# Kernel tuning notes

Measured on AMD Instinct MI355X. Metric: run time of the kernel, lower is better.

## Reference

```python
import jax, jax.numpy as jnp
import numpy as np

ALPHA = 0.2
NEG_INF = -9e15


def setup_inputs() -> dict:
    key = jax.random.key(0)
    k1, k2, k3, k4 = jax.random.split(key, 4)
    B, N, Fin, Fout = 8, 2048, 128, 64
    h = jax.random.normal(k1, (B, N, Fin), dtype=jnp.float32)
    adj = jax.random.randint(k2, (N, N), 0, 2, dtype=jnp.int32)
    # xavier-uniform-ish scale for params
    W = jax.random.normal(k3, (Fin, Fout), dtype=jnp.float32) * (1.414 * (2.0 / (Fin + Fout)) ** 0.5)
    a = jax.random.normal(k4, (2 * Fout, 1), dtype=jnp.float32) * (1.414 * (2.0 / (2 * Fout + 1)) ** 0.5)
    return {"h": h, "adj": adj, "W": W, "a": a}


def reference(h, adj, W, a):
    # h: [B,N,Fin], adj: [N,N] int, W: [Fin,Fout], a: [2*Fout,1]
    Wh = jnp.matmul(h, W)                       # [B,N,F]
    Fout = W.shape[1]
    a1 = a[:Fout, 0]                            # attends to source node i
    a2 = a[Fout:, 0]                            # attends to target node j
    # e[b,i,j] = leakyrelu(Wh[b,i]·a1 + Wh[b,j]·a2)  (no [B,N,N,2F] tensor)
    si = jnp.einsum('bnf,f->bn', Wh, a1)        # [B,N]
    sj = jnp.einsum('bnf,f->bn', Wh, a2)        # [B,N]
    e = si[:, :, None] + sj[:, None, :]         # [B,N,N]
    e = jnp.where(e > 0, e, ALPHA * e)          # leaky_relu
    mask = (adj > 0)[None, :, :]                # [1,N,N] broadcast over batch
    attention = jax.nn.softmax(jnp.where(mask, e, NEG_INF), axis=2)
    h_prime = jnp.matmul(attention, Wh)         # [B,N,F]
    return jax.nn.elu(h_prime), attention
```

## Files before the change

### kernel.cpp

```cpp
#include <hip/hip_runtime.h>
#include <hip/hip_bf16.h>
#include <string.h>

constexpr int B_ = 8;
constexpr int N_ = 2048;
constexpr int FIN = 128;
constexpr int FOUT = 64;
constexpr float ALPHA_ = 0.2f;
constexpr float NEG_INF_ = -9000000000000000.0f;

typedef __attribute__((ext_vector_type(8))) short bf16x8;
typedef __attribute__((ext_vector_type(4))) float f32x4;

static __device__ __forceinline__ unsigned short f2bf(float x) {
  unsigned int u = __float_as_uint(x);
  unsigned int r = u + 0x7fffu + ((u >> 16) & 1u);
  return (unsigned short)(r >> 16);
}

__global__ __launch_bounds__(256) void k_wh(
    const float* __restrict__ h, const float* __restrict__ W,
    const float* __restrict__ a, unsigned short* __restrict__ WhT,
    float* __restrict__ si, float* __restrict__ sj) {
  const int lane = threadIdx.x & 63;
  const int wv = threadIdx.x >> 6;
  const int grow0 = blockIdx.x * 32 + wv * 8;
  const int f = lane;
  float acc[8] = {0.f, 0.f, 0.f, 0.f, 0.f, 0.f, 0.f, 0.f};
  const float* hp = h + (size_t)grow0 * FIN;
#pragma unroll 4
  for (int k = 0; k < FIN; k += 4) {
    float w0 = W[k * FOUT + f];
    float w1 = W[(k + 1) * FOUT + f];
    float w2 = W[(k + 2) * FOUT + f];
    float w3 = W[(k + 3) * FOUT + f];
#pragma unroll
    for (int r = 0; r < 8; ++r) {
      float4 hv = *(const float4*)(hp + r * FIN + k);
      acc[r] = fmaf(hv.x, w0, acc[r]);
      acc[r] = fmaf(hv.y, w1, acc[r]);
      acc[r] = fmaf(hv.z, w2, acc[r]);
      acc[r] = fmaf(hv.w, w3, acc[r]);
    }
  }
  const float a1 = a[f], a2 = a[FOUT + f];
#pragma unroll
  for (int r = 0; r < 8; ++r) {
    float p1 = acc[r] * a1;
    float p2 = acc[r] * a2;
#pragma unroll
    for (int off = 32; off; off >>= 1) {
      p1 += __shfl_xor(p1, off);
      p2 += __shfl_xor(p2, off);
    }
    if (lane == 0) {
      si[grow0 + r] = p1;
      sj[grow0 + r] = p2;
    }
  }
  const int b = grow0 >> 11;
  const int n0 = grow0 & (N_ - 1);
  __align__(16) unsigned short u[8];
#pragma unroll
  for (int r = 0; r < 8; ++r) u[r] = f2bf(acc[r]);
  *(bf16x8*)&WhT[(((size_t)(b * FOUT + f)) << 11) + n0] = *(const bf16x8*)u;
}

__global__ __launch_bounds__(256) void k_pack(
    const int* __restrict__ adj, unsigned long long* __restrict__ mask_rm,
    unsigned int* __restrict__ mask_t) {
  const int lane = threadIdx.x & 63;
  const int wv = threadIdx.x >> 6;
  const int r = blockIdx.x * 4 + wv;
  const int* row = adj + (size_t)r * N_;
  unsigned int wacc = 0;
#pragma unroll
  for (int it = 0; it < 32; ++it) {
    int v = row[it * 64 + lane];
    unsigned long long bm = __ballot(v > 0);
    if (lane == 0) mask_rm[r * 32 + it] = bm;
    wacc |= ((unsigned int)(v > 0)) << it;
  }
  mask_t[r * 64 + lane] = wacc;
}

__global__ __launch_bounds__(256) void k_stats(
    const unsigned int* __restrict__ mask_t, const float* __restrict__ si,
    const float* __restrict__ sj, float* __restrict__ mrow,
    float* __restrict__ rrow) {
  const int lane = threadIdx.x & 63;
  const int wv = threadIdx.x >> 6;
  const int row = blockIdx.x * 4 + wv;
  const int b = row >> 11;
  const int i = row & (N_ - 1);
  const unsigned int w32 = mask_t[i * 64 + lane];
  const float* sjb = sj + ((size_t)b << 11);
  float sjv[32];
  float M = -3.0e38f;
#pragma unroll
  for (int it = 0; it < 32; ++it) {
    sjv[it] = sjb[it * 64 + lane];
    if ((w32 >> it) & 1u) M = fmaxf(M, sjv[it]);
  }
#pragma unroll
  for (int off = 32; off; off >>= 1) M = fmaxf(M, __shfl_xor(M, off));
  const float siv = si[row];
  const float e0 = siv + M;
  const float m = e0 > 0.f ? e0 : ALPHA_ * e0;
  float s = 0.f;
#pragma unroll
  for (int it = 0; it < 32; ++it) {
    float e = siv + sjv[it];
    float v = e > 0.f ? e : ALPHA_ * e;
    float p = __expf(v - m);
    s += ((w32 >> it) & 1u) ? p : 0.f;
  }
#pragma unroll
  for (int off = 32; off; off >>= 1) s += __shfl_xor(s, off);
  if (lane == 0) {
    mrow[row] = m;
    rrow[row] = 1.f / s;
  }
}

constexpr int TI = 32;

__global__ __launch_bounds__(512, 4) void k_hp(
    const unsigned short* __restrict__ WhT,
    const unsigned long long* __restrict__ mask_rm,
    const float* __restrict__ si, const float* __restrict__ sjg,
    const float* __restrict__ mrow, const float* __restrict__ rrow,
    float* __restrict__ h_out) {
  __shared__ float red[4][TI][FOUT];

  const int bid = blockIdx.x;
  const int swz = (bid & 7) * 64 + (bid >> 3);
  const int b = swz >> 6;
  const int i0 = (swz & 63) * TI;

  const int tid = threadIdx.x;
  const int lane = tid & 63;
  const int wv = tid >> 6;
  const int rl = lane & 15;
  const int hi = lane >> 4;
  const int jsl = wv * 256;

  const int grow0 = (b << 11) + i0 + rl;
  const int grow1 = grow0 + 16;
  const float sir0 = si[grow0], sir1 = si[grow1];
  const float mK0 = mrow[grow0] * 1.44269504f, mK1 = mrow[grow1] * 1.44269504f;
  const float rr0 = rrow[grow0], rr1 = rrow[grow1];
  const float* __restrict__ sjb = sjg + ((size_t)b << 11);

  const unsigned char* maskb = (const unsigned char*)mask_rm;
  const uint4 mA0 = *(const uint4*)(maskb + (i0 + rl) * 256 + (jsl >> 3));
  const uint4 mA1 = *(const uint4*)(maskb + (i0 + rl) * 256 + (jsl >> 3) + 16);
  const uint4 mB0 = *(const uint4*)(maskb + (i0 + 16 + rl) * 256 + (jsl >> 3));
  const uint4 mB1 = *(const uint4*)(maskb + (i0 + 16 + rl) * 256 + (jsl >> 3) + 16);
  const unsigned int mw0[8] = {mA0.x, mA0.y, mA0.z, mA0.w, mA1.x, mA1.y, mA1.z, mA1.w};
  const unsigned int mw1[8] = {mB0.x, mB0.y, mB0.z, mB0.w, mB1.x, mB1.y, mB1.z, mB1.w};

  const unsigned short* wbp[4];
#pragma unroll
  for (int ct = 0; ct < 4; ++ct)
    wbp[ct] = WhT + (((size_t)(b * FOUT + ct * 16 + rl)) << 11) + jsl + hi * 8;

  f32x4 acc[2][4];
#pragma unroll
  for (int rt = 0; rt < 2; ++rt)
#pragma unroll
    for (int ct = 0; ct < 4; ++ct) acc[rt][ct] = (f32x4){0.f, 0.f, 0.f, 0.f};

#pragma unroll
  for (int ks = 0; ks < 8; ++ks) {
    const int jb = jsl + ks * 32 + hi * 8;
    const float4 s0 = *(const float4*)(sjb + jb);
    const float4 s1 = *(const float4*)(sjb + jb + 4);
    const float sjl[8] = {s0.x, s0.y, s0.z, s0.w, s1.x, s1.y, s1.z, s1.w};

    bf16x8 afr0, afr1;
    {
      const unsigned int mby = (mw0[ks] >> (hi * 8)) & 0xffu;
      __align__(16) unsigned short u[8];
#pragma unroll
      for (int e = 0; e < 8; ++e) {
        float ev = sir0 + sjl[e];
        float v = fmaxf(ev, ALPHA_ * ev);
        float p = exp2f(fmaf(v, 1.44269504f, -mK0)) * rr0;
        u[e] = ((mby >> e) & 1u) ? f2bf(p) : 0;
      }
      afr0 = *(const bf16x8*)u;
    }
    {
      const unsigned int mby = (mw1[ks] >> (hi * 8)) & 0xffu;
      __align__(16) unsigned short u[8];
#pragma unroll
      for (int e = 0; e < 8; ++e) {
        float ev = sir1 + sjl[e];
        float v = fmaxf(ev, ALPHA_ * ev);
        float p = exp2f(fmaf(v, 1.44269504f, -mK1)) * rr1;
        u[e] = ((mby >> e) & 1u) ? f2bf(p) : 0;
      }
      afr1 = *(const bf16x8*)u;
    }

#pragma unroll
    for (int ct = 0; ct < 4; ++ct) {
      bf16x8 bv = *(const bf16x8*)(wbp[ct] + ks * 32);
      acc[0][ct] = __builtin_amdgcn_mfma_f32_16x16x32_bf16(afr0, bv, acc[0][ct], 0, 0, 0);
      acc[1][ct] = __builtin_amdgcn_mfma_f32_16x16x32_bf16(afr1, bv, acc[1][ct], 0, 0, 0);
    }
  }

  if (wv < 4) {
#pragma unroll
    for (int rt = 0; rt < 2; ++rt)
#pragma unroll
      for (int ct = 0; ct < 4; ++ct)
#pragma unroll
        for (int rg = 0; rg < 4; ++rg)
          red[wv][rt * 16 + hi * 4 + rg][ct * 16 + rl] = acc[rt][ct][rg];
  }
  __syncthreads();
  if (wv >= 4) {
#pragma unroll
    for (int rt = 0; rt < 2; ++rt)
#pragma unroll
      for (int ct = 0; ct < 4; ++ct)
#pragma unroll
        for (int rg = 0; rg < 4; ++rg)
          red[wv - 4][rt * 16 + hi * 4 + rg][ct * 16 + rl] += acc[rt][ct][rg];
  }
  __syncthreads();

#pragma unroll
  for (int k = tid; k < TI * FOUT; k += 512) {
    const int r = k >> 6;
    const int c = k & 63;
    float x = red[0][r][c] + red[1][r][c] + red[2][r][c] + red[3][r][c];
    float o = x > 0.f ? x : __expf(x) - 1.f;
    h_out[(((size_t)((b << 11) + i0 + r)) << 6) + c] = o;
  }
}

__global__ __launch_bounds__(256) void k_att(
    const unsigned char* __restrict__ maskb, const float* __restrict__ si,
    const float* __restrict__ sjg, const float* __restrict__ mrow,
    const float* __restrict__ rrow, float* __restrict__ att_out) {
  const int lane = threadIdx.x & 63;
  const int wv = threadIdx.x >> 6;
  const int row = blockIdx.x * 4 + wv;
  const int b = row >> 11;
  const int i = row & (N_ - 1);
  const float sir = si[row];
  const float mK = mrow[row] * 1.44269504f;
  const float rr = rrow[row];
  const float* __restrict__ sjb = sjg + ((size_t)b << 11);
  const unsigned char* __restrict__ mb = maskb + i * 256;
  float* __restrict__ ao = att_out + ((size_t)row << 11);

#pragma unroll
  for (int it = 0; it < 8; ++it) {
    const int j = it * 256 + lane * 4;
    const float4 s = *(const float4*)(sjb + j);
    const unsigned int mby = mb[it * 32 + (lane >> 1)] >> ((lane & 1) * 4);
    const float sjl[4] = {s.x, s.y, s.z, s.w};
    float av[4];
#pragma unroll
    for (int e = 0; e < 4; ++e) {
      float ev = sir + sjl[e];
      float v = fmaxf(ev, ALPHA_ * ev);
      float p = exp2f(fmaf(v, 1.44269504f, -mK)) * rr;
      av[e] = ((mby >> e) & 1u) ? p : 0.f;
    }
    f32x4 vv = {av[0], av[1], av[2], av[3]};
    *(f32x4*)(ao + j) = vv;
  }
}

extern "C" void kernel_launch(void* const* d_in, const int* in_sizes, int n_in,
                              void* d_out, int out_size, void* d_ws, size_t ws_size,
                              hipStream_t stream) {
  const float* h = (const float*)d_in[0];
  const int* adj = (const int*)d_in[1];
  const float* W = (const float*)d_in[2];
  const float* a = (const float*)d_in[3];

  float* out = (float*)d_out;
  float* h_out = out;
  float* att_out = out + (size_t)B_ * N_ * FOUT;

  unsigned short* WhT = (unsigned short*)d_ws;
  float* si = (float*)((char*)d_ws + (size_t)2 * 1024 * 1024);
  float* sj = si + B_ * N_;
  float* mrow = sj + B_ * N_;
  float* rrow = mrow + B_ * N_;
  unsigned long long* mask_rm = (unsigned long long*)(rrow + B_ * N_);
  unsigned int* mask_t = (unsigned int*)((char*)mask_rm + (size_t)N_ * 32 * 8);

  k_wh<<<B_ * N_ / 32, 256, 0, stream>>>(h, W, a, WhT, si, sj);
  k_pack<<<N_ / 4, 256, 0, stream>>>(adj, mask_rm, mask_t);
  k_stats<<<B_ * N_ / 4, 256, 0, stream>>>(mask_t, si, sj, mrow, rrow);
  k_hp<<<B_ * (N_ / TI), 512, 0, stream>>>(WhT, mask_rm, si, sj, mrow, rrow,
                                           h_out);
  k_att<<<B_ * N_ / 4, 256, 0, stream>>>((const unsigned char*)mask_rm, si, sj,
                                         mrow, rrow, att_out);
}
```

Before: 97.96 us.

## Compute h_prime by reading the written attention matrix instead of recomputing probabilities

The fused k_hp kernel, which recomputed masked softmax probabilities on the fly before the MFMA product, is removed. A new k_gemm kernel runs after k_att, reads the fp32 attention output from global memory, converts it to bf16 and multiplies it with WhT. This removes the duplicated exp and mask work but adds a 128 MB read of the attention matrix, which is likely to be served partly from cache, plus a serial dependency on k_att.

```diff
diff --git a/kernel.cpp b/kernel.cpp
--- a/kernel.cpp
+++ b/kernel.cpp
@@ -123,126 +123,6 @@
   }
 }
 
-constexpr int TI = 32;
-
-__global__ __launch_bounds__(512, 4) void k_hp(
-    const unsigned short* __restrict__ WhT,
-    const unsigned long long* __restrict__ mask_rm,
-    const float* __restrict__ si, const float* __restrict__ sjg,
-    const float* __restrict__ mrow, const float* __restrict__ rrow,
-    float* __restrict__ h_out) {
-  __shared__ float red[4][TI][FOUT];
-
-  const int bid = blockIdx.x;
-  const int swz = (bid & 7) * 64 + (bid >> 3);
-  const int b = swz >> 6;
-  const int i0 = (swz & 63) * TI;
-
-  const int tid = threadIdx.x;
-  const int lane = tid & 63;
-  const int wv = tid >> 6;
-  const int rl = lane & 15;
-  const int hi = lane >> 4;
-  const int jsl = wv * 256;
-
-  const int grow0 = (b << 11) + i0 + rl;
-  const int grow1 = grow0 + 16;
-  const float sir0 = si[grow0], sir1 = si[grow1];
-  const float mK0 = mrow[grow0] * 1.44269504f, mK1 = mrow[grow1] * 1.44269504f;
-  const float rr0 = rrow[grow0], rr1 = rrow[grow1];
-  const float* __restrict__ sjb = sjg + ((size_t)b << 11);
-
-  const unsigned char* maskb = (const unsigned char*)mask_rm;
-  const uint4 mA0 = *(const uint4*)(maskb + (i0 + rl) * 256 + (jsl >> 3));
-  const uint4 mA1 = *(const uint4*)(maskb + (i0 + rl) * 256 + (jsl >> 3) + 16);
-  const uint4 mB0 = *(const uint4*)(maskb + (i0 + 16 + rl) * 256 + (jsl >> 3));
-  const uint4 mB1 = *(const uint4*)(maskb + (i0 + 16 + rl) * 256 + (jsl >> 3) + 16);
-  const unsigned int mw0[8] = {mA0.x, mA0.y, mA0.z, mA0.w, mA1.x, mA1.y, mA1.z, mA1.w};
-  const unsigned int mw1[8] = {mB0.x, mB0.y, mB0.z, mB0.w, mB1.x, mB1.y, mB1.z, mB1.w};
-
-  const unsigned short* wbp[4];
-#pragma unroll
-  for (int ct = 0; ct < 4; ++ct)
-    wbp[ct] = WhT + (((size_t)(b * FOUT + ct * 16 + rl)) << 11) + jsl + hi * 8;
-
-  f32x4 acc[2][4];
-#pragma unroll
-  for (int rt = 0; rt < 2; ++rt)
-#pragma unroll
-    for (int ct = 0; ct < 4; ++ct) acc[rt][ct] = (f32x4){0.f, 0.f, 0.f, 0.f};
-
-#pragma unroll
-  for (int ks = 0; ks < 8; ++ks) {
-    const int jb = jsl + ks * 32 + hi * 8;
-    const float4 s0 = *(const float4*)(sjb + jb);
-    const float4 s1 = *(const float4*)(sjb + jb + 4);
-    const float sjl[8] = {s0.x, s0.y, s0.z, s0.w, s1.x, s1.y, s1.z, s1.w};
-
-    bf16x8 afr0, afr1;
-    {
-      const unsigned int mby = (mw0[ks] >> (hi * 8)) & 0xffu;
-      __align__(16) unsigned short u[8];
-#pragma unroll
-      for (int e = 0; e < 8; ++e) {
-        float ev = sir0 + sjl[e];
-        float v = fmaxf(ev, ALPHA_ * ev);
-        float p = exp2f(fmaf(v, 1.44269504f, -mK0)) * rr0;
-        u[e] = ((mby >> e) & 1u) ? f2bf(p) : 0;
-      }
-      afr0 = *(const bf16x8*)u;
-    }
-    {
-      const unsigned int mby = (mw1[ks] >> (hi * 8)) & 0xffu;
-      __align__(16) unsigned short u[8];
-#pragma unroll
-      for (int e = 0; e < 8; ++e) {
-        float ev = sir1 + sjl[e];
-        float v = fmaxf(ev, ALPHA_ * ev);
-        float p = exp2f(fmaf(v, 1.44269504f, -mK1)) * rr1;
-        u[e] = ((mby >> e) & 1u) ? f2bf(p) : 0;
-      }
-      afr1 = *(const bf16x8*)u;
-    }
-
-#pragma unroll
-    for (int ct = 0; ct < 4; ++ct) {
-      bf16x8 bv = *(const bf16x8*)(wbp[ct] + ks * 32);
-      acc[0][ct] = __builtin_amdgcn_mfma_f32_16x16x32_bf16(afr0, bv, acc[0][ct], 0, 0, 0);
-      acc[1][ct] = __builtin_amdgcn_mfma_f32_16x16x32_bf16(afr1, bv, acc[1][ct], 0, 0, 0);
-    }
-  }
-
-  if (wv < 4) {
-#pragma unroll
-    for (int rt = 0; rt < 2; ++rt)
-#pragma unroll
-      for (int ct = 0; ct < 4; ++ct)
-#pragma unroll
-        for (int rg = 0; rg < 4; ++rg)
-          red[wv][rt * 16 + hi * 4 + rg][ct * 16 + rl] = acc[rt][ct][rg];
-  }
-  __syncthreads();
-  if (wv >= 4) {
-#pragma unroll
-    for (int rt = 0; rt < 2; ++rt)
-#pragma unroll
-      for (int ct = 0; ct < 4; ++ct)
-#pragma unroll
-        for (int rg = 0; rg < 4; ++rg)
-          red[wv - 4][rt * 16 + hi * 4 + rg][ct * 16 + rl] += acc[rt][ct][rg];
-  }
-  __syncthreads();
-
-#pragma unroll
-  for (int k = tid; k < TI * FOUT; k += 512) {
-    const int r = k >> 6;
-    const int c = k & 63;
-    float x = red[0][r][c] + red[1][r][c] + red[2][r][c] + red[3][r][c];
-    float o = x > 0.f ? x : __expf(x) - 1.f;
-    h_out[(((size_t)((b << 11) + i0 + r)) << 6) + c] = o;
-  }
-}
-
 __global__ __launch_bounds__(256) void k_att(
     const unsigned char* __restrict__ maskb, const float* __restrict__ si,
     const float* __restrict__ sjg, const float* __restrict__ mrow,
@@ -278,6 +158,79 @@
   }
 }
 
+__global__ __launch_bounds__(512, 4) void k_gemm(
+    const float* __restrict__ att, const unsigned short* __restrict__ WhT,
+    float* __restrict__ h_out) {
+  __shared__ float red[4][16][FOUT];
+
+  const int bid = blockIdx.x;
+  const int swz = (bid & 7) * 64 + (bid >> 3);
+  const int b = swz >> 6;
+  const int i0 = (swz & 63) * 32;
+
+  const int tid = threadIdx.x;
+  const int lane = tid & 63;
+  const int wv = tid >> 6;
+  const int rt = wv >> 2;
+  const int kw = wv & 3;
+  const int rl = lane & 15;
+  const int hi = lane >> 4;
+
+  const float* __restrict__ arow =
+      att + (((size_t)((b << 11) + i0 + rt * 16 + rl)) << 11) + kw * 512 + hi * 8;
+  const unsigned short* wb[4];
+#pragma unroll
+  for (int ct = 0; ct < 4; ++ct)
+    wb[ct] = WhT + (((size_t)(b * FOUT + ct * 16 + rl)) << 11) + kw * 512 + hi * 8;
+
+  f32x4 acc[4];
+#pragma unroll
+  for (int ct = 0; ct < 4; ++ct) acc[ct] = (f32x4){0.f, 0.f, 0.f, 0.f};
+
+#pragma unroll 4
+  for (int ks = 0; ks < 16; ++ks) {
+    const float4 a0 = *(const float4*)(arow + ks * 32);
+    const float4 a1 = *(const float4*)(arow + ks * 32 + 4);
+    __align__(16) unsigned short u[8];
+    u[0] = f2bf(a0.x); u[1] = f2bf(a0.y); u[2] = f2bf(a0.z); u[3] = f2bf(a0.w);
+    u[4] = f2bf(a1.x); u[5] = f2bf(a1.y); u[6] = f2bf(a1.z); u[7] = f2bf(a1.w);
+    const bf16x8 af = *(const bf16x8*)u;
+#pragma unroll
+    for (int ct = 0; ct < 4; ++ct) {
+      bf16x8 bv = *(const bf16x8*)(wb[ct] + ks * 32);
+      acc[ct] = __builtin_amdgcn_mfma_f32_16x16x32_bf16(af, bv, acc[ct], 0, 0, 0);
+    }
+  }
+
+  if (kw < 2) {
+#pragma unroll
+    for (int ct = 0; ct < 4; ++ct)
+#pragma unroll
+      for (int rg = 0; rg < 4; ++rg)
+        red[rt * 2 + kw][hi * 4 + rg][ct * 16 + rl] = acc[ct][rg];
+  }
+  __syncthreads();
+  if (kw >= 2) {
+#pragma unroll
+    for (int ct = 0; ct < 4; ++ct)
+#pragma unroll
+      for (int rg = 0; rg < 4; ++rg)
+        red[rt * 2 + (kw - 2)][hi * 4 + rg][ct * 16 + rl] += acc[ct][rg];
+  }
+  __syncthreads();
+
+#pragma unroll
+  for (int k = tid; k < 32 * FOUT; k += 512) {
+    const int r = k >> 6;
+    const int c = k & 63;
+    const int rt2 = r >> 4;
+    const int rr2 = r & 15;
+    float x = red[rt2 * 2][rr2][c] + red[rt2 * 2 + 1][rr2][c];
+    float o = x > 0.f ? x : __expf(x) - 1.f;
+    h_out[(((size_t)((b << 11) + i0 + r)) << 6) + c] = o;
+  }
+}
+
 extern "C" void kernel_launch(void* const* d_in, const int* in_sizes, int n_in,
                               void* d_out, int out_size, void* d_ws, size_t ws_size,
                               hipStream_t stream) {
@@ -301,8 +254,7 @@
   k_wh<<<B_ * N_ / 32, 256, 0, stream>>>(h, W, a, WhT, si, sj);
   k_pack<<<N_ / 4, 256, 0, stream>>>(adj, mask_rm, mask_t);
   k_stats<<<B_ * N_ / 4, 256, 0, stream>>>(mask_t, si, sj, mrow, rrow);
-  k_hp<<<B_ * (N_ / TI), 512, 0, stream>>>(WhT, mask_rm, si, sj, mrow, rrow,
-                                           h_out);
   k_att<<<B_ * N_ / 4, 256, 0, stream>>>((const unsigned char*)mask_rm, si, sj,
                                          mrow, rrow, att_out);
-}
+  k_gemm<<<B_ * (N_ / 32), 512, 0, stream>>>(att_out, WhT, h_out);
+}
```

New measurement: 119.2 us. 21.7% more time.
